# Kernel optimization log

Measured on AMD Instinct MI355X. Metric: run time of the kernel, lower is better.

## Reference

```python
import jax, jax.numpy as jnp
import numpy as np


def _haar_dwt(x):
    # pywt 'haar' dwt2 on even-sized inputs: non-overlapping 2x2 blocks.
    # For block [[a,b],[c,d]]: cA=(a+b+c+d)/2, cH=(a+b-c-d)/2,
    # cV=(a-b+c-d)/2, cD=(a-b-c+d)/2  (pywt dec_hi = [-1/sqrt2, 1/sqrt2]).
    B, C, H, W = x.shape
    xb = x.reshape(B, C, H // 2, 2, W // 2, 2)
    a = xb[:, :, :, 0, :, 0]
    b = xb[:, :, :, 0, :, 1]
    c = xb[:, :, :, 1, :, 0]
    d = xb[:, :, :, 1, :, 1]
    ll = (a + b + c + d) * 0.5
    ch = (a + b - c - d) * 0.5
    cv = (a - b + c - d) * 0.5
    cd = (a - b - c + d) * 0.5
    return ll, ch, cv, cd


def _haar_idwt(ll, ch, cv, cd):
    a = (ll + ch + cv + cd) * 0.5
    b = (ll + ch - cv - cd) * 0.5
    c = (ll - ch + cv - cd) * 0.5
    d = (ll - ch - cv + cd) * 0.5
    B, C, h2, w2 = ll.shape
    top = jnp.stack([a, b], axis=-1)   # [B,C,h2,w2,2]
    bot = jnp.stack([c, d], axis=-1)   # [B,C,h2,w2,2]
    y = jnp.stack([top, bot], axis=-3)  # [B,C,h2,2,w2,2]
    return y.reshape(B, C, 2 * h2, 2 * w2)


def _conv2d(x, w, b, groups=1, pad=1):
    y = jax.lax.conv_general_dilated(
        x, w, window_strides=(1, 1), padding=[(pad, pad), (pad, pad)],
        dimension_numbers=('NCHW', 'OIHW', 'NCHW'), feature_group_count=groups)
    return y + b[None, :, None, None]


def setup_inputs() -> dict:
    key = jax.random.key(0)
    ks = jax.random.split(key, 7)
    B, C, H, W = 8, 64, 256, 256
    C4 = 4 * C
    x = jax.random.normal(ks[0], (B, C, H, W), dtype=jnp.float32)
    dw_w = jax.random.normal(ks[1], (C4, 1, 3, 3), dtype=jnp.float32) / 3.0
    dw_b = jax.random.normal(ks[2], (C4,), dtype=jnp.float32) * 0.01
    pw_w = jax.random.normal(ks[3], (C4, C4, 1, 1), dtype=jnp.float32) / float(np.sqrt(C4))
    pw_b = jax.random.normal(ks[4], (C4,), dtype=jnp.float32) * 0.01
    cv_w = jax.random.normal(ks[5], (C4, C4, 3, 3), dtype=jnp.float32) / float(3.0 * np.sqrt(C4))
    cv_b = jax.random.normal(ks[6], (C4,), dtype=jnp.float32) * 0.01
    return {"x": x, "dw_w": dw_w, "dw_b": dw_b, "pw_w": pw_w,
            "pw_b": pw_b, "cv_w": cv_w, "cv_b": cv_b}


def reference(x, dw_w, dw_b, pw_w, pw_b, cv_w, cv_b):
    B, C, H, W = x.shape  # source math requires H == W (spatial transpose)
    C4 = 4 * C
    ll, ch, cv, cd = _haar_dwt(x)
    # Source stores each subband spatially TRANSPOSED (transpose(2,1,0)).
    sub = jnp.stack([jnp.swapaxes(s, -1, -2) for s in (ll, ch, cv, cd)], axis=2)
    t = sub.reshape(B, C4, H // 2, W // 2)  # channel order c*4 + {LL,cH,cV,cD}
    t = _conv2d(t, dw_w, dw_b, groups=C4, pad=1)  # depthwise 3x3
    t = _conv2d(t, pw_w, pw_b, groups=1, pad=0)   # pointwise 1x1
    t = _conv2d(t, cv_w, cv_b, groups=1, pad=1)   # dense 3x3
    t = jax.nn.gelu(t, approximate=False)         # torch nn.GELU() = exact erf
    t = t.reshape(B, C, 4, H // 2, W // 2)
    # Inverse path un-transposes each subband (transpose(0,2) in source).
    ll2, ch2, cv2, cd2 = [jnp.swapaxes(t[:, :, k], -1, -2) for k in range(4)]
    return _haar_idwt(ll2, ch2, cv2, cd2)
```

## Files before the change

kernel.cpp:

```cpp
#include <hip/hip_runtime.h>
#include <hip/hip_bf16.h>

#define DEVI __device__ __forceinline__

typedef __attribute__((ext_vector_type(8))) short abf8;
typedef __attribute__((ext_vector_type(4))) float f32x4;

DEVI unsigned short f2bf(float f) {
  union { __hip_bfloat16 h; unsigned short u; } cvt;
  cvt.h = __float2bfloat16(f);
  return cvt.u;
}
DEVI float bf2f(unsigned short u) {
  return __uint_as_float(((unsigned)u) << 16);
}
DEVI void async16(const void* g, void* l) {
  __builtin_amdgcn_global_load_lds((__attribute__((address_space(1))) void*)(g),
                                   (__attribute__((address_space(3))) void*)(l), 16, 0, 0);
}

__global__ __launch_bounds__(256) void k0_prep(const float* __restrict__ pw_w,
                                               const float* __restrict__ cv_w,
                                               unsigned short* __restrict__ pwb,
                                               unsigned short* __restrict__ cvb) {
  int id = blockIdx.x * 256 + threadIdx.x;
  if (id < 65536) pwb[id] = f2bf(pw_w[id]);
  if (id < 589824) {
    int dd = id >> 16;
    int rem = id & 65535;
    cvb[id] = f2bf(cv_w[(size_t)rem * 9 + dd]);
  }
}

__global__ __launch_bounds__(256) void k1a_dwt(const float* __restrict__ x,
                                               unsigned short* __restrict__ t0) {
  __shared__ __align__(16) float L[64 * 65];
  const int t = threadIdx.x;
  const int u0 = (blockIdx.x & 3) * 32;
  const int v0 = (blockIdx.x >> 2) * 32;
  const int c = blockIdx.y, b = blockIdx.z;
  const float* xp = x + (((size_t)(b * 64 + c)) << 16);
  {
    const int row = t >> 2;
    const float* xr = xp + (size_t)(2 * v0 + row) * 256 + 2 * u0;
    float* Lr = L + row * 65;
    for (int j = 0; j < 4; ++j) {
      int col = ((t & 3) + j * 4) * 4;
      float4 val = *(const float4*)(xr + col);
      Lr[col] = val.x; Lr[col + 1] = val.y; Lr[col + 2] = val.z; Lr[col + 3] = val.w;
    }
  }
  __syncthreads();
  const int vv = t & 31;
  const int us = t >> 5;
  const size_t outc = ((size_t)(b * 256 + c * 4)) << 14;
  for (int pass = 0; pass < 4; ++pass) {
    int uu = us * 4 + pass;
    const float* Lp = L + (2 * vv) * 65 + 2 * uu;
    float a = Lp[0], bb = Lp[1], cc = Lp[65], dd = Lp[66];
    float sll = (a + bb + cc + dd) * 0.5f;
    float sch = (a + bb - cc - dd) * 0.5f;
    float scv = (a - bb + cc - dd) * 0.5f;
    float scd = (a - bb - cc + dd) * 0.5f;
    size_t base = outc + ((u0 + uu) << 7) + (v0 + vv);
    t0[base]         = f2bf(sll);
    t0[base + 16384] = f2bf(sch);
    t0[base + 32768] = f2bf(scv);
    t0[base + 49152] = f2bf(scd);
  }
}

__global__ __launch_bounds__(256) void k1b_dw(const unsigned short* __restrict__ t0,
                                              const float* __restrict__ dww,
                                              const float* __restrict__ dwb,
                                              unsigned short* __restrict__ t1) {
  __shared__ __align__(16) unsigned short S[32 * 181];
  __shared__ __align__(16) unsigned short O[128 * 32];
  const int t = threadIdx.x;
  const int u0 = (blockIdx.x >> 3) * 8;
  const int v0 = (blockIdx.x & 7) * 16;
  const int icB = blockIdx.y * 32;
  const int b = blockIdx.z;
  const unsigned short* t0b = t0 + (((size_t)(b * 256 + icB)) << 14);
  for (int idx = t; idx < 5760; idx += 256) {
    int ic = idx / 180;
    int r = idx - ic * 180;
    int uu = r / 18;
    int vvq = r - uu * 18;
    int gu = u0 + uu - 1, gv = v0 + vvq - 1;
    unsigned short val = 0;
    if ((unsigned)gu < 128u && (unsigned)gv < 128u)
      val = t0b[((size_t)ic << 14) + (gu << 7) + gv];
    S[ic * 181 + r] = val;
  }
  __syncthreads();
  const int icp = t & 15, uu = (t >> 4) & 7, vh = t >> 7;
  const int cc0 = icB + icp * 2;
  float w0[9], w1[9];
  const float* wp = dww + cc0 * 9;
  for (int i = 0; i < 9; ++i) { w0[i] = wp[i]; w1[i] = wp[9 + i]; }
  const float b0 = dwb[cc0], b1 = dwb[cc0 + 1];
  const unsigned short* S0 = S + (icp * 2) * 181 + uu * 18 + vh * 8;
  const unsigned short* S1 = S0 + 181;
  float a0[3][3], a1[3][3];
  for (int du = 0; du < 3; ++du)
    for (int dv = 0; dv < 2; ++dv) {
      a0[du][dv] = bf2f(S0[du * 18 + dv]);
      a1[du][dv] = bf2f(S1[du * 18 + dv]);
    }
  unsigned* O32 = (unsigned*)O;
  for (int vv = 0; vv < 8; ++vv) {
    for (int du = 0; du < 3; ++du) {
      a0[du][2] = bf2f(S0[du * 18 + vv + 2]);
      a1[du][2] = bf2f(S1[du * 18 + vv + 2]);
    }
    float s0 = b0, s1 = b1;
    for (int du = 0; du < 3; ++du)
      for (int dv = 0; dv < 3; ++dv) {
        s0 += w0[du * 3 + dv] * a0[du][dv];
        s1 += w1[du * 3 + dv] * a1[du][dv];
      }
    int p = uu * 16 + vh * 8 + vv;
    O32[p * 16 + icp] = (unsigned)f2bf(s0) | ((unsigned)f2bf(s1) << 16);
    for (int du = 0; du < 3; ++du) {
      a0[du][0] = a0[du][1]; a0[du][1] = a0[du][2];
      a1[du][0] = a1[du][1]; a1[du][1] = a1[du][2];
    }
  }
  __syncthreads();
  const int p = t >> 1, hf = t & 1;
  const int pu = p >> 4, pv = p & 15;
  size_t gp = (size_t)((u0 + pu) * 128 + (v0 + pv));
  const uint4* src = (const uint4*)(O + p * 32 + hf * 16);
  uint4* dst = (uint4*)(t1 + ((((size_t)b * 16384) + gp) << 8) + icB + hf * 16);
  dst[0] = src[0];
  dst[1] = src[1];
}

__global__ __launch_bounds__(256) void k2_pw(const unsigned short* __restrict__ t1,
                                             const unsigned short* __restrict__ pwb,
                                             const float* __restrict__ pw_bias,
                                             unsigned short* __restrict__ t2) {
  __shared__ __align__(16) char smem[34816];
  unsigned short* As = (unsigned short*)smem;
  unsigned short* Bs = (unsigned short*)(smem + 8192);
  unsigned short* Ost = (unsigned short*)smem;
  const int t = threadIdx.x;
  const int wv = t >> 6, ln = t & 63;
  const int p0 = blockIdx.x * 128;
  const int oc0 = blockIdx.y * 128;
  const int b = blockIdx.z;
  const unsigned short* t1b = t1 + ((size_t)b << 22);
  const int q = ln >> 4, cl = ln & 15;
  const int lr = ln >> 2, sp = ln & 3;
  const int sc = (sp - (lr >> 1)) & 3;
  const int soff = ((q + (cl >> 1)) & 3) * 8;
  f32x4 acc[2][8] = {};
  for (int ic0 = 0; ic0 < 256; ic0 += 32) {
    __syncthreads();
    for (int cpy = 0; cpy < 2; ++cpy) {
      int rb = wv * 32 + cpy * 16;
      async16(pwb + (((size_t)(oc0 + rb + lr)) << 8) + ic0 + sc * 8, As + rb * 32);
      async16(t1b + (((size_t)(p0 + rb + lr)) << 8) + ic0 + sc * 8, Bs + rb * 32);
    }
    __syncthreads();
    abf8 a0 = *(const abf8*)(As + (wv * 32 + cl) * 32 + soff);
    abf8 a1 = *(const abf8*)(As + (wv * 32 + 16 + cl) * 32 + soff);
    for (int nt = 0; nt < 8; ++nt) {
      abf8 bf = *(const abf8*)(Bs + (nt * 16 + cl) * 32 + soff);
      acc[0][nt] = __builtin_amdgcn_mfma_f32_16x16x32_bf16(a0, bf, acc[0][nt], 0, 0, 0);
      acc[1][nt] = __builtin_amdgcn_mfma_f32_16x16x32_bf16(a1, bf, acc[1][nt], 0, 0, 0);
    }
  }
  __syncthreads();
  for (int mt = 0; mt < 2; ++mt) {
    int ocr = wv * 32 + mt * 16 + q * 4;
    float bb0 = pw_bias[oc0 + ocr],     bb1 = pw_bias[oc0 + ocr + 1];
    float bb2 = pw_bias[oc0 + ocr + 2], bb3 = pw_bias[oc0 + ocr + 3];
    for (int nt = 0; nt < 8; ++nt) {
      int p = nt * 16 + cl;
      short4 pk;
      pk.x = (short)f2bf(acc[mt][nt][0] + bb0);
      pk.y = (short)f2bf(acc[mt][nt][1] + bb1);
      pk.z = (short)f2bf(acc[mt][nt][2] + bb2);
      pk.w = (short)f2bf(acc[mt][nt][3] + bb3);
      *(short4*)(Ost + p * 136 + ocr) = pk;
    }
  }
  __syncthreads();
  const int pr = t >> 1, hf = t & 1;
  const uint4* src = (const uint4*)(Ost + pr * 136 + hf * 64);
  uint4* dst = (uint4*)(t2 + (((size_t)(b * 16384 + p0 + pr)) << 8) + oc0 + hf * 64);
  for (int j = 0; j < 8; ++j) dst[j] = src[j];
}

__global__ __launch_bounds__(256) void k3_cv(const unsigned short* __restrict__ t2,
                                             const unsigned short* __restrict__ cvb,
                                             const float* __restrict__ cv_bias,
                                             unsigned short* __restrict__ t3) {
  __shared__ __align__(16) char smem[34816];
  unsigned short* As = (unsigned short*)smem;
  unsigned short* Bs = (unsigned short*)(smem + 24576);
  unsigned short* Ost = (unsigned short*)smem;
  const int t = threadIdx.x;
  const int wv = t >> 6, ln = t & 63;
  const int oc0 = blockIdx.x * 128;
  const int u = blockIdx.y;
  const int b = blockIdx.z;
  const unsigned short* t2b = t2 + ((size_t)b << 22);
  const int q = ln >> 4, cl = ln & 15;
  const int lr = ln >> 2, sp = ln & 3;
  const int scA = (sp - (lr >> 1)) & 3;
  const int scB = (sp - ((1 + lr) >> 1)) & 3;
  const int soffA = ((q + (cl >> 1)) & 3) * 8;
  if (t < 32) ((unsigned*)Bs)[t < 16 ? t : (2064 + (t - 16))] = 0;
  f32x4 acc[2][8] = {};
  for (int du = 0; du < 3; ++du) {
    const int us = u + du - 1;
    if ((unsigned)us >= 128u) continue;
    const unsigned short* trow = t2b + ((size_t)us << 15);
    const unsigned short* wdu = cvb + (((size_t)(du * 3)) << 16);
    for (int ic0 = 0; ic0 < 256; ic0 += 32) {
      __syncthreads();
      for (int g = wv; g < 32; g += 4) {
        if (g < 24) {
          int dv = g >> 3, ch = g & 7;
          async16(wdu + (((size_t)dv) << 16) + (((size_t)(oc0 + ch * 16 + lr)) << 8) + ic0 + scA * 8,
                  As + dv * 4096 + ch * 512);
        } else {
          int ch = g - 24;
          async16(trow + (((size_t)(ch * 16 + lr)) << 8) + ic0 + scB * 8,
                  Bs + 32 + ch * 512);
        }
      }
      __syncthreads();
      for (int dv = 0; dv < 3; ++dv) {
        const unsigned short* Adv = As + dv * 4096;
        abf8 a0 = *(const abf8*)(Adv + (wv * 32 + cl) * 32 + soffA);
        abf8 a1 = *(const abf8*)(Adv + (wv * 32 + 16 + cl) * 32 + soffA);
        const int slotB = ((q + ((cl + dv) >> 1)) & 3) * 8;
        const unsigned short* Bbase = Bs + (cl + dv) * 32 + slotB;
        for (int nt = 0; nt < 8; ++nt) {
          abf8 bf = *(const abf8*)(Bbase + nt * 512);
          acc[0][nt] = __builtin_amdgcn_mfma_f32_16x16x32_bf16(a0, bf, acc[0][nt], 0, 0, 0);
          acc[1][nt] = __builtin_amdgcn_mfma_f32_16x16x32_bf16(a1, bf, acc[1][nt], 0, 0, 0);
        }
      }
    }
  }
  __syncthreads();
  for (int mt = 0; mt < 2; ++mt) {
    int ocr = wv * 32 + mt * 16 + q * 4;
    for (int r = 0; r < 4; ++r) {
      float bias = cv_bias[oc0 + ocr + r];
      for (int nt = 0; nt < 8; ++nt) {
        float xv = acc[mt][nt][r] + bias;
        float u_ = 0.7978845608028654f * xv * (1.0f + 0.044715f * xv * xv);
        float e = __expf(-2.0f * fabsf(u_));
        float th = (1.0f - e) / (1.0f + e);
        th = (u_ >= 0.0f) ? th : -th;
        float g = 0.5f * xv * (1.0f + th);
        Ost[(ocr + r) * 136 + nt * 16 + cl] = f2bf(g);
      }
    }
  }
  __syncthreads();
  const int rr = t >> 1, hf = t & 1;
  const uint4* src = (const uint4*)(Ost + rr * 136 + hf * 64);
  uint4* dst = (uint4*)(t3 + ((size_t)(b * 256 + oc0 + rr) << 14) + (u << 7) + hf * 64);
  for (int j = 0; j < 8; ++j) dst[j] = src[j];
}

__global__ __launch_bounds__(256) void k4_idwt(const unsigned short* __restrict__ t3,
                                               float* __restrict__ out) {
  __shared__ __align__(16) unsigned short L[4 * 32 * 34];
  const int t = threadIdx.x;
  const int w20 = (blockIdx.x & 3) * 32;
  const int h20 = (blockIdx.x >> 2) * 32;
  const int c = blockIdx.y, b = blockIdx.z;
  const unsigned short* t3b = t3 + (((size_t)(b * 256 + c * 4)) << 14);
  {
    const int row = t >> 1, hf = t & 1;
    const int k = row >> 5, w2i = row & 31;
    const unsigned* g = (const unsigned*)(t3b + ((size_t)k << 14) + ((w20 + w2i) << 7) + h20 + hf * 16);
    unsigned* l = (unsigned*)(L + (k * 32 + w2i) * 34 + hf * 16);
    for (int j = 0; j < 8; ++j) l[j] = g[j];
  }
  __syncthreads();
  const int w2 = t & 31;
  const int h2b = t >> 5;
  float* ob = out + (((size_t)(b * 64 + c)) << 16);
  for (int pass = 0; pass < 4; ++pass) {
    int h2 = h2b + pass * 8;
    int off = w2 * 34 + h2;
    float ll = bf2f(L[off]);
    float ch = bf2f(L[off + 1088]);
    float cv = bf2f(L[off + 2176]);
    float cd = bf2f(L[off + 3264]);
    float A  = (ll + ch + cv + cd) * 0.5f;
    float Bv = (ll + ch - cv - cd) * 0.5f;
    float Cv = (ll - ch + cv - cd) * 0.5f;
    float D  = (ll - ch - cv + cd) * 0.5f;
    int hg = (h20 + h2) * 2, wg = (w20 + w2) * 2;
    *(float2*)(ob + (size_t)hg * 256 + wg)       = make_float2(A, Bv);
    *(float2*)(ob + (size_t)(hg + 1) * 256 + wg) = make_float2(Cv, D);
  }
}

extern "C" void kernel_launch(void* const* d_in, const int* in_sizes, int n_in,
                              void* d_out, int out_size, void* d_ws, size_t ws_size,
                              hipStream_t stream) {
  const float* x    = (const float*)d_in[0];
  const float* dw_w = (const float*)d_in[1];
  const float* dw_b = (const float*)d_in[2];
  const float* pw_w = (const float*)d_in[3];
  const float* pw_b = (const float*)d_in[4];
  const float* cv_w = (const float*)d_in[5];
  const float* cv_b = (const float*)d_in[6];
  char* ws = (char*)d_ws;
  unsigned short* pwb  = (unsigned short*)(ws + 4096);
  unsigned short* cvb  = (unsigned short*)(ws + 4096 + 131072);
  unsigned short* bufA = (unsigned short*)(ws + (size_t)(2u << 20));
  unsigned short* bufB = (unsigned short*)(ws + (size_t)(70u << 20));
  k0_prep<<<2304, 256, 0, stream>>>(pw_w, cv_w, pwb, cvb);
  k1a_dwt<<<dim3(16, 64, 8), 256, 0, stream>>>(x, bufA);
  k1b_dw<<<dim3(128, 8, 8), 256, 0, stream>>>(bufA, dw_w, dw_b, bufB);
  k2_pw<<<dim3(128, 2, 8), 256, 0, stream>>>(bufB, pwb, pw_b, bufA);
  k3_cv<<<dim3(2, 128, 8), 256, 0, stream>>>(bufA, cvb, cv_b, bufB);
  k4_idwt<<<dim3(16, 64, 8), 256, 0, stream>>>(bufB, (float*)d_out);
}
```

Baseline: 565.1 us.

## Compute two output rows per block in dense conv with 32x32x16 MFMA tiles

The dense 3x3 conv kernel now has each block produce two output rows (128 oc x 256 pixels) instead of one. It stages the four needed input rows in LDS once per input-channel chunk and reuses them across the three kernel rows and both output rows. The MFMA shape moves from 16x16x32 to 32x32x16, the loop order becomes ic-outer/du-inner, and the epilogue writes the two rows in phases. This halves input-row reloads and raises compute per LDS read, at the cost of more LDS (occupancy hint of 2) and more registers for the larger accumulators.

```diff
diff --git a/kernel.cpp b/kernel.cpp
--- a/kernel.cpp
+++ b/kernel.cpp
@@ -5,6 +5,7 @@
 
 typedef __attribute__((ext_vector_type(8))) short abf8;
 typedef __attribute__((ext_vector_type(4))) float f32x4;
+typedef __attribute__((ext_vector_type(16))) float f32x16;
 
 DEVI unsigned short f2bf(float f) {
   union { __hip_bfloat16 h; unsigned short u; } cvt;
@@ -194,81 +195,102 @@
   for (int j = 0; j < 8; ++j) dst[j] = src[j];
 }
 
-__global__ __launch_bounds__(256) void k3_cv(const unsigned short* __restrict__ t2,
-                                             const unsigned short* __restrict__ cvb,
-                                             const float* __restrict__ cv_bias,
-                                             unsigned short* __restrict__ t3) {
-  __shared__ __align__(16) char smem[34816];
+__global__ __launch_bounds__(256, 2) void k3_cv(const unsigned short* __restrict__ t2,
+                                                const unsigned short* __restrict__ cvb,
+                                                const float* __restrict__ cv_bias,
+                                                unsigned short* __restrict__ t3) {
+  __shared__ __align__(16) char smem[57856];
   unsigned short* As = (unsigned short*)smem;
   unsigned short* Bs = (unsigned short*)(smem + 24576);
   unsigned short* Ost = (unsigned short*)smem;
   const int t = threadIdx.x;
   const int wv = t >> 6, ln = t & 63;
+  const int wm = wv & 1, wn = wv >> 1;
   const int oc0 = blockIdx.x * 128;
-  const int u = blockIdx.y;
+  const int u0r = blockIdx.y * 2;
   const int b = blockIdx.z;
   const unsigned short* t2b = t2 + ((size_t)b << 22);
-  const int q = ln >> 4, cl = ln & 15;
+  for (int i = t; i < 8320; i += 256) ((unsigned*)Bs)[i] = 0;
   const int lr = ln >> 2, sp = ln & 3;
-  const int scA = (sp - (lr >> 1)) & 3;
-  const int scB = (sp - ((1 + lr) >> 1)) & 3;
-  const int soffA = ((q + (cl >> 1)) & 3) * 8;
-  if (t < 32) ((unsigned*)Bs)[t < 16 ? t : (2064 + (t - 16))] = 0;
-  f32x4 acc[2][8] = {};
-  for (int du = 0; du < 3; ++du) {
-    const int us = u + du - 1;
-    if ((unsigned)us >= 128u) continue;
-    const unsigned short* trow = t2b + ((size_t)us << 15);
-    const unsigned short* wdu = cvb + (((size_t)(du * 3)) << 16);
-    for (int ic0 = 0; ic0 < 256; ic0 += 32) {
+  const int cB = (sp - ((1 + lr) >> 1)) & 3;
+  const int cA = (sp - (lr >> 1)) & 3;
+  const int usB = u0r - 1 + wv;
+  const bool okB = (unsigned)usB < 128u;
+  const unsigned short* gB0 = t2b + (((size_t)(usB < 0 ? 0 : usB)) << 15) + lr * 256 + cB * 8;
+  const unsigned short* gA0 = cvb + (size_t)(oc0 + wv * 16 + lr) * 256 + cA * 8;
+  const int l5 = ln >> 5, lm = ln & 31;
+  const int segA0 = ((l5 + (lm >> 1)) & 3) * 8;
+  f32x16 acc[2][4] = {};
+  for (int ic0 = 0; ic0 < 256; ic0 += 32) {
+    for (int du = 0; du < 3; ++du) {
       __syncthreads();
-      for (int g = wv; g < 32; g += 4) {
-        if (g < 24) {
-          int dv = g >> 3, ch = g & 7;
-          async16(wdu + (((size_t)dv) << 16) + (((size_t)(oc0 + ch * 16 + lr)) << 8) + ic0 + scA * 8,
-                  As + dv * 4096 + ch * 512);
-        } else {
-          int ch = g - 24;
-          async16(trow + (((size_t)(ch * 16 + lr)) << 8) + ic0 + scB * 8,
-                  Bs + 32 + ch * 512);
+      if (du == 0 && okB) {
+        const unsigned short* g = gB0 + ic0;
+        unsigned short* ld = Bs + wv * 4160 + 32;
+#pragma unroll
+        for (int s = 0; s < 8; ++s) async16(g + s * 4096, ld + s * 512);
+      }
+      {
+        const unsigned short* g = gA0 + (size_t)(du * 3) * 65536 + ic0;
+#pragma unroll
+        for (int s = 0; s < 6; ++s) {
+          const int dv = s >> 1, half = s & 1;
+          async16(g + dv * 65536 + half * 16384,
+                  As + dv * 4096 + (wv + half * 4) * 512);
         }
       }
       __syncthreads();
+#pragma unroll
       for (int dv = 0; dv < 3; ++dv) {
         const unsigned short* Adv = As + dv * 4096;
-        abf8 a0 = *(const abf8*)(Adv + (wv * 32 + cl) * 32 + soffA);
-        abf8 a1 = *(const abf8*)(Adv + (wv * 32 + 16 + cl) * 32 + soffA);
-        const int slotB = ((q + ((cl + dv) >> 1)) & 3) * 8;
-        const unsigned short* Bbase = Bs + (cl + dv) * 32 + slotB;
-        for (int nt = 0; nt < 8; ++nt) {
-          abf8 bf = *(const abf8*)(Bbase + nt * 512);
-          acc[0][nt] = __builtin_amdgcn_mfma_f32_16x16x32_bf16(a0, bf, acc[0][nt], 0, 0, 0);
-          acc[1][nt] = __builtin_amdgcn_mfma_f32_16x16x32_bf16(a1, bf, acc[1][nt], 0, 0, 0);
+        const int rb = lm + dv;
+        const int segB0 = ((l5 + (rb >> 1)) & 3) * 8;
+        const unsigned short* Bb = Bs + (wn + du) * 4160 + rb * 32;
+#pragma unroll
+        for (int kk = 0; kk < 2; ++kk) {
+          const int sA = segA0 ^ (kk * 16);
+          const int sB = segB0 ^ (kk * 16);
+          abf8 a0 = *(const abf8*)(Adv + (wm * 64 + lm) * 32 + sA);
+          abf8 a1 = *(const abf8*)(Adv + (wm * 64 + 32 + lm) * 32 + sA);
+#pragma unroll
+          for (int nt = 0; nt < 4; ++nt) {
+            abf8 bf = *(const abf8*)(Bb + nt * 1024 + sB);
+            acc[0][nt] = __builtin_amdgcn_mfma_f32_32x32x16_bf16(a0, bf, acc[0][nt], 0, 0, 0);
+            acc[1][nt] = __builtin_amdgcn_mfma_f32_32x32x16_bf16(a1, bf, acc[1][nt], 0, 0, 0);
+          }
         }
       }
     }
   }
-  __syncthreads();
-  for (int mt = 0; mt < 2; ++mt) {
-    int ocr = wv * 32 + mt * 16 + q * 4;
-    for (int r = 0; r < 4; ++r) {
-      float bias = cv_bias[oc0 + ocr + r];
-      for (int nt = 0; nt < 8; ++nt) {
-        float xv = acc[mt][nt][r] + bias;
-        float u_ = 0.7978845608028654f * xv * (1.0f + 0.044715f * xv * xv);
-        float e = __expf(-2.0f * fabsf(u_));
-        float th = (1.0f - e) / (1.0f + e);
-        th = (u_ >= 0.0f) ? th : -th;
-        float g = 0.5f * xv * (1.0f + th);
-        Ost[(ocr + r) * 136 + nt * 16 + cl] = f2bf(g);
-      }
-    }
-  }
-  __syncthreads();
-  const int rr = t >> 1, hf = t & 1;
-  const uint4* src = (const uint4*)(Ost + rr * 136 + hf * 64);
-  uint4* dst = (uint4*)(t3 + ((size_t)(b * 256 + oc0 + rr) << 14) + (u << 7) + hf * 64);
-  for (int j = 0; j < 8; ++j) dst[j] = src[j];
+#pragma unroll
+  for (int ph = 0; ph < 2; ++ph) {
+    __syncthreads();
+    if (wn == ph) {
+#pragma unroll
+      for (int mt = 0; mt < 2; ++mt)
+#pragma unroll
+        for (int reg = 0; reg < 16; ++reg) {
+          const int ocr = wm * 64 + mt * 32 + (reg & 3) + 8 * (reg >> 2) + 4 * l5;
+          const float bias = cv_bias[oc0 + ocr];
+#pragma unroll
+          for (int nt = 0; nt < 4; ++nt) {
+            float xv = acc[mt][nt][reg] + bias;
+            float u_ = 0.7978845608028654f * xv * (1.0f + 0.044715f * xv * xv);
+            float e = __expf(-2.0f * fabsf(u_));
+            float th = (1.0f - e) / (1.0f + e);
+            th = (u_ >= 0.0f) ? th : -th;
+            float g = 0.5f * xv * (1.0f + th);
+            Ost[ocr * 136 + nt * 32 + lm] = f2bf(g);
+          }
+        }
+    }
+    __syncthreads();
+    const int rr = t >> 1, hf = t & 1;
+    const uint4* src = (const uint4*)(Ost + rr * 136 + hf * 64);
+    uint4* dst = (uint4*)(t3 + ((size_t)(b * 256 + oc0 + rr) << 14) + ((u0r + ph) << 7) + hf * 64);
+#pragma unroll
+    for (int j = 0; j < 8; ++j) dst[j] = src[j];
+  }
 }
 
 __global__ __launch_bounds__(256) void k4_idwt(const unsigned short* __restrict__ t3,
@@ -326,6 +348,6 @@
   k1a_dwt<<<dim3(16, 64, 8), 256, 0, stream>>>(x, bufA);
   k1b_dw<<<dim3(128, 8, 8), 256, 0, stream>>>(bufA, dw_w, dw_b, bufB);
   k2_pw<<<dim3(128, 2, 8), 256, 0, stream>>>(bufB, pwb, pw_b, bufA);
-  k3_cv<<<dim3(2, 128, 8), 256, 0, stream>>>(bufA, cvb, cv_b, bufB);
+  k3_cv<<<dim3(2, 64, 8), 256, 0, stream>>>(bufA, cvb, cv_b, bufB);
   k4_idwt<<<dim3(16, 64, 8), 256, 0, stream>>>(bufB, (float*)d_out);
 }
```

Measured after the change: 571.3 us. About the same (+1.1%).
